# Optimization experiments

Hardware: AMD Instinct MI355X
Metric: run time of the kernel (lower is better)

## Reference

```python
import jax, jax.numpy as jnp
import numpy as np

DIM = 768
HEADS = 8
HIDDEN = 3072
B, Hs, Ws = 16, 32, 32
N = Hs * Ws
LN_EPS = 1e-5


def setup_inputs() -> dict:
    key = jax.random.key(0)
    ks = jax.random.split(key, 10)
    s = lambda *sh: 0.02
    return {
        "x": jax.random.normal(ks[0], (B, N, DIM), jnp.float32),
        "Wq": jax.random.normal(ks[1], (DIM, DIM), jnp.float32) * 0.02,
        "temperature": jnp.ones((HEADS, 1, 1), jnp.float32),
        "fc1_w": jax.random.normal(ks[2], (HIDDEN, DIM), jnp.float32) * 0.02,
        "fc1_b": jnp.zeros((HIDDEN,), jnp.float32),
        "dw_w": jax.random.normal(ks[3], (HIDDEN, 1, 3, 3), jnp.float32) * 0.1,
        "dw_b": jnp.zeros((HIDDEN,), jnp.float32),
        "gamma": jnp.ones((HIDDEN,), jnp.float32),
        "fc2_w": jax.random.normal(ks[4], (DIM, HIDDEN), jnp.float32) * 0.02,
        "fc2_b": jnp.zeros((DIM,), jnp.float32),
        "ln_w": jnp.ones((DIM,), jnp.float32),
        "ln_b": jnp.zeros((DIM,), jnp.float32),
        "H": Hs,
        "W": Ws,
    }


def _dwconv(x, w, b, H, W):
    # x: (B, N, hidden) -> depthwise 3x3, pad 1 -> (B, N, hidden)
    Bn, Nn, Ch = x.shape
    img = x.transpose(0, 2, 1).reshape(Bn, Ch, H, W)
    out = jax.lax.conv_general_dilated(
        img, w, window_strides=(1, 1), padding=((1, 1), (1, 1)),
        dimension_numbers=("NCHW", "OIHW", "NCHW"), feature_group_count=Ch)
    out = out + b[None, :, None, None]
    return out.reshape(Bn, Ch, Nn).transpose(0, 2, 1)


def _layernorm(x, w, b):
    mu = x.mean(-1, keepdims=True)
    var = ((x - mu) ** 2).mean(-1, keepdims=True)
    return (x - mu) * jax.lax.rsqrt(var + LN_EPS) * w + b


def reference(x, Wq, temperature, fc1_w, fc1_b, dw_w, dw_b, gamma,
              fc2_w, fc2_b, ln_w, ln_b, H, W):
    # gpd_ratio == active_ratio == 1 -> pre/post scalings cancel
    Bn, Nn, C = x.shape
    h = temperature.shape[0]
    Ch = C // h
    # q/k/v heads: (B, h, N, Ch)
    q = (x @ Wq.T).reshape(Bn, Nn, h, Ch).transpose(0, 2, 1, 3)
    kv = x.reshape(Bn, Nn, h, Ch).transpose(0, 2, 1, 3)
    # channel attention: softmax over N, pool k over Ch, sigmoid gate
    qs = jax.nn.softmax(q, axis=-2).transpose(0, 1, 3, 2)      # (B,h,Ch,N)
    kp = jax.nn.softmax(kv, axis=-2).mean(-1, keepdims=True)    # (B,h,N,1)
    attn = jax.nn.sigmoid(qs @ kp) * temperature                # (B,h,Ch,1)
    # MLP on v (== x after scaling cancels): fc1 -> dwconv residual -> fc2 -> LN
    h1 = x @ fc1_w.T + fc1_b                                    # (B,N,hidden)
    h2 = gamma * _dwconv(h1, dw_w, dw_b, H, W) + h1
    v = _layernorm(h2 @ fc2_w.T + fc2_b, ln_w, ln_b)            # (B,N,C)
    v = v.reshape(Bn, Nn, h, Ch).transpose(0, 2, 1, 3)          # (B,h,N,Ch)
    prod = attn * v.transpose(0, 1, 3, 2)                       # (B,h,Ch,N)
    out = prod.transpose(0, 3, 1, 2).reshape(Bn, Nn, C)
    return out, prod.transpose(0, 1, 3, 2)
```

## Files before the change

### kernel.cpp

```cpp
#include <hip/hip_runtime.h>

#define BATCH 16
#define SEQ   1024
#define DIM   768
#define NHEAD 8
#define CHD   96
#define HID   3072
#define MTOT  (BATCH * SEQ)

using u16 = unsigned short;
typedef __attribute__((ext_vector_type(8))) short bf16x8;
typedef __attribute__((ext_vector_type(4))) float f32x4;

#define AS1 __attribute__((address_space(1)))
#define AS3 __attribute__((address_space(3)))

__device__ inline float bf2f(u16 u) {
    union { unsigned int i; float f; } v; v.i = ((unsigned int)u) << 16; return v.f;
}
__device__ inline u16 f2bf(float f) {
    union { float f; unsigned int i; } v; v.f = f;
    unsigned int r = v.i + 0x7FFFu + ((v.i >> 16) & 1u);
    return (u16)(r >> 16);
}

__device__ inline void gld16(const void* g, void* l) {
    __builtin_amdgcn_global_load_lds((AS1 const void*)g, (AS3 void*)l, 16, 0, 0);
}

template <int BM>
__global__ __launch_bounds__(512) void gemm_p(const u16* __restrict__ A,
                                              const u16* __restrict__ B,
                                              const float* __restrict__ bias,
                                              u16* __restrict__ C1, int N1,
                                              u16* __restrict__ C2,
                                              int M, int N, int K) {
    constexpr int AROUNDS = BM / 128;
    constexpr int GPT = 2 + AROUNDS;
    constexpr int ASLOT = BM * 32;
    constexpr int AFOLD = BM / 2;
    constexpr int NFI = BM / 32;
    __shared__ u16 lds[4 * (ASLOT + 8192)];

    const int tid = threadIdx.x;
    const int lane = tid & 63;
    const int wid = tid >> 6;
    const int wm = (wid >> 2) * (BM / 2);
    const int wn = (wid & 3) << 6;

    const int nwg = gridDim.x;
    const int wg = blockIdx.x;
    const int lid = (wg & 7) * (nwg >> 3) + (wg >> 3);
    const int nbx = N >> 8;
    const int mb = lid / nbx, nb = lid - mb * nbx;
    const int m0 = mb * BM, n0 = nb << 8;

    const int sprow = tid >> 3;
    const int s_l = (tid & 7) ^ (sprow & 7);
    const int sgk = (s_l & 3) << 3;
    const u16* pa = A + (size_t)(m0 + (s_l >> 2) * AFOLD + sprow) * K + sgk;
    const u16* pb = B + (size_t)(n0 + (s_l >> 2) * 128 + sprow) * K + sgk;
    const size_t r64K = (size_t)64 * K;

#define STAGE_A(slot, k0) do {                                        \
    gld16(pa + (k0), &lds[(slot) * (ASLOT + 8192) + tid * 8]);        \
    if (AROUNDS == 2)                                                 \
        gld16(pa + (k0) + r64K,                                       \
              &lds[(slot) * (ASLOT + 8192) + 4096 + tid * 8]);        \
} while (0)
#define STAGE_B(slot, k0) do {                                        \
    gld16(pb + (k0), &lds[(slot) * (ASLOT + 8192) + ASLOT + tid * 8]);\
    gld16(pb + (k0) + r64K,                                           \
          &lds[(slot) * (ASLOT + 8192) + ASLOT + 4096 + tid * 8]);    \
} while (0)

    const int lrow = lane & 15;
    const int kg = lane >> 4;
    const int xA = (((wid >> 2) * 4 + kg) ^ (lrow & 7)) << 3;
    const int xB = (((wn >> 7) * 4 + kg) ^ (lrow & 7)) << 3;
    const int bbase = (wn & 64) + lrow;

    f32x4 acc[NFI][4] = {};

    const int NT = K >> 5;
    STAGE_A(0, 0);  STAGE_B(0, 0);
    STAGE_A(1, 32); STAGE_B(1, 32);
    STAGE_A(2, 64); STAGE_B(2, 64);

    for (int t = 0; t < NT; ++t) {
        const int rem = NT - 1 - t;
        if (rem >= 2) {
            if constexpr (GPT == 4) asm volatile("s_waitcnt vmcnt(8)" ::: "memory");
            else                    asm volatile("s_waitcnt vmcnt(6)" ::: "memory");
        } else if (rem == 1) {
            if constexpr (GPT == 4) asm volatile("s_waitcnt vmcnt(4)" ::: "memory");
            else                    asm volatile("s_waitcnt vmcnt(3)" ::: "memory");
        } else {
            asm volatile("s_waitcnt vmcnt(0)" ::: "memory");
        }
        __builtin_amdgcn_sched_barrier(0);
        __builtin_amdgcn_s_barrier();

        const u16* Ls = &lds[(t & 3) * (ASLOT + 8192)];
        const int k3 = (t + 3) << 5;

        bf16x8 bfr[4], af[NFI / 2];
#pragma unroll
        for (int j = 0; j < 4; ++j)
            bfr[j] = *(const bf16x8*)&Ls[ASLOT + (bbase + j * 16) * 64 + xB];
#pragma unroll
        for (int i = 0; i < NFI / 2; ++i)
            af[i] = *(const bf16x8*)&Ls[(i * 16 + lrow) * 64 + xA];
        if (rem >= 3) STAGE_A((t + 3) & 3, k3);
        asm volatile("s_waitcnt lgkmcnt(0)" ::: "memory");
        __builtin_amdgcn_sched_barrier(0);
        __builtin_amdgcn_s_setprio(1);
#pragma unroll
        for (int i = 0; i < NFI / 2; ++i)
#pragma unroll
            for (int j = 0; j < 4; ++j)
                acc[i][j] = __builtin_amdgcn_mfma_f32_16x16x32_bf16(af[i], bfr[j], acc[i][j], 0, 0, 0);
        __builtin_amdgcn_s_setprio(0);
        __builtin_amdgcn_s_barrier();

        bf16x8 af2[NFI / 2];
#pragma unroll
        for (int i = 0; i < NFI / 2; ++i)
            af2[i] = *(const bf16x8*)&Ls[((i + NFI / 2) * 16 + lrow) * 64 + xA];
        if (rem >= 3) STAGE_B((t + 3) & 3, k3);
        asm volatile("s_waitcnt lgkmcnt(0)" ::: "memory");
        __builtin_amdgcn_sched_barrier(0);
        __builtin_amdgcn_s_setprio(1);
#pragma unroll
        for (int i = 0; i < NFI / 2; ++i)
#pragma unroll
            for (int j = 0; j < 4; ++j)
                acc[i + NFI / 2][j] = __builtin_amdgcn_mfma_f32_16x16x32_bf16(af2[i], bfr[j], acc[i + NFI / 2][j], 0, 0, 0);
        __builtin_amdgcn_s_setprio(0);
    }
#undef STAGE_A
#undef STAGE_B

    const int crow = (lane >> 4) << 2, ccol = lane & 15;
    const int N2 = N - N1;
#pragma unroll
    for (int i = 0; i < NFI; ++i) {
        const int gm = m0 + wm + i * 16 + crow;
#pragma unroll
        for (int j = 0; j < 4; ++j) {
            const int gn = n0 + wn + j * 16 + ccol;
            if (gn < N1) {
                const float bv = bias ? bias[gn] : 0.f;
#pragma unroll
                for (int r = 0; r < 4; ++r)
                    C1[(size_t)(gm + r) * N1 + gn] = f2bf(acc[i][j][r] + bv);
            } else {
#pragma unroll
                for (int r = 0; r < 4; ++r)
                    C2[(size_t)(gm + r) * N2 + gn - N1] = f2bf(acc[i][j][r]);
            }
        }
    }
}

__global__ __launch_bounds__(256) void cvt_all(const float* __restrict__ x,
                                               const float* __restrict__ Wq,
                                               const float* __restrict__ w1,
                                               const float* __restrict__ w2,
                                               u16* __restrict__ xb,
                                               u16* __restrict__ Wqb,
                                               u16* __restrict__ w1b,
                                               u16* __restrict__ w2b) {
    const int E0 = MTOT * DIM / 4;
    const int E1 = E0 + DIM * DIM / 4;
    const int E2 = E1 + HID * DIM / 4;
    const int E3 = E2 + DIM * HID / 4;
    int i = blockIdx.x * 256 + threadIdx.x;
    if (i >= E3) return;
    const float* in; u16* out; int k;
    if (i < E0)      { in = x;  out = xb;  k = i; }
    else if (i < E1) { in = Wq; out = Wqb; k = i - E0; }
    else if (i < E2) { in = w1; out = w1b; k = i - E1; }
    else             { in = w2; out = w2b; k = i - E2; }
    float4 v = reinterpret_cast<const float4*>(in)[k];
    ushort4 o;
    o.x = f2bf(v.x); o.y = f2bf(v.y); o.z = f2bf(v.z); o.w = f2bf(v.w);
    reinterpret_cast<ushort4*>(out)[k] = o;
}

__global__ __launch_bounds__(256) void colsm_stats(const u16* __restrict__ X,
                                                   float* __restrict__ Mo,
                                                   float* __restrict__ So) {
    const int tid = threadIdx.x, lane = tid & 63, chunk = tid >> 6;
    const int b = blockIdx.y;
    const int j = blockIdx.x * 64 + lane;
    const u16* p = X + (size_t)b * SEQ * DIM + j;
    float m = -3.0e38f, s = 0.f;
    const int nEnd = (chunk + 1) << 8;
    for (int n = chunk << 8; n < nEnd; ++n) {
        float raw = bf2f(p[(size_t)n * DIM]);
        float nm = fmaxf(m, raw);
        s = s * __expf(m - nm) + __expf(raw - nm);
        m = nm;
    }
    __shared__ float ms[4][64], ss[4][64];
    ms[chunk][lane] = m; ss[chunk][lane] = s;
    __syncthreads();
    if (tid < 64) {
        float M = fmaxf(fmaxf(ms[0][lane], ms[1][lane]), fmaxf(ms[2][lane], ms[3][lane]));
        float S = ss[0][lane] * __expf(ms[0][lane] - M) + ss[1][lane] * __expf(ms[1][lane] - M) +
                  ss[2][lane] * __expf(ms[2][lane] - M) + ss[3][lane] * __expf(ms[3][lane] - M);
        Mo[b * DIM + j] = M;
        So[b * DIM + j] = S;
    }
}

__global__ __launch_bounds__(256) void kp_k(const u16* __restrict__ x,
                                            const float* __restrict__ Mx,
                                            const float* __restrict__ Sx,
                                            float* __restrict__ kp) {
    const int n = blockIdx.x, b = blockIdx.y, tid = threadIdx.x;
    __shared__ float p[DIM];
    const u16* row = x + ((size_t)b * SEQ + n) * DIM;
#pragma unroll
    for (int q = 0; q < 3; ++q) {
        int j = tid + (q << 8);
        p[j] = __expf(bf2f(row[j]) - Mx[b * DIM + j]) / Sx[b * DIM + j];
    }
    __syncthreads();
    if (tid < NHEAD) {
        float s = 0.f;
        for (int c = 0; c < CHD; ++c) s += p[tid * CHD + c];
        kp[((size_t)b * NHEAD + tid) * SEQ + n] = s * (1.f / (float)CHD);
    }
}

__global__ __launch_bounds__(256) void qattn_k(const u16* __restrict__ Q,
                                               const float* __restrict__ kp,
                                               const float* __restrict__ temp,
                                               float* __restrict__ attnv) {
    const int tid = threadIdx.x, lane = tid & 63, chunk = tid >> 6;
    const int b = blockIdx.y;
    const int j = blockIdx.x * 64 + lane;
    const int h = j / CHD;
    const u16* qp = Q + (size_t)b * SEQ * DIM + j;
    const float* kpp = kp + ((size_t)b * NHEAD + h) * SEQ;
    float m = -3.0e38f, s = 0.f, a = 0.f;
    const int nEnd = (chunk + 1) << 8;
    for (int n = chunk << 8; n < nEnd; ++n) {
        float q = bf2f(qp[(size_t)n * DIM]);
        float nm = fmaxf(m, q);
        float sc = __expf(m - nm), e = __expf(q - nm);
        s = s * sc + e;
        a = a * sc + e * kpp[n];
        m = nm;
    }
    __shared__ float ms[4][64], ss[4][64], as_[4][64];
    ms[chunk][lane] = m; ss[chunk][lane] = s; as_[chunk][lane] = a;
    __syncthreads();
    if (tid < 64) {
        float M = fmaxf(fmaxf(ms[0][lane], ms[1][lane]), fmaxf(ms[2][lane], ms[3][lane]));
        float S = 0.f, A = 0.f;
#pragma unroll
        for (int c = 0; c < 4; ++c) {
            float sc = __expf(ms[c][lane] - M);
            S += ss[c][lane] * sc;
            A += as_[c][lane] * sc;
        }
        float z = A / S;
        attnv[b * DIM + j] = temp[h] / (1.f + __expf(-z));
    }
}

__global__ __launch_bounds__(128) void dwconv_v(const u16* __restrict__ h1,
                                                const float* __restrict__ w,
                                                const float* __restrict__ dwb,
                                                const float* __restrict__ gamma,
                                                u16* __restrict__ h2) {
    const int g = blockIdx.x * 128 + threadIdx.x;
    const int y = blockIdx.y >> 2;
    const int xw0 = (blockIdx.y & 3) << 3;
    const int b = blockIdx.z;
    const int ch0 = g << 3;

    float wreg[8][9], bias2[8];
#pragma unroll
    for (int c = 0; c < 8; ++c) {
        const float gm = gamma[ch0 + c];
#pragma unroll
        for (int k = 0; k < 9; ++k) wreg[c][k] = gm * w[(ch0 + c) * 9 + k];
        wreg[c][4] += 1.0f;
        bias2[c] = gm * dwb[ch0 + c];
    }

    float acc[8][8];
#pragma unroll
    for (int xo = 0; xo < 8; ++xo)
#pragma unroll
        for (int c = 0; c < 8; ++c) acc[xo][c] = bias2[c];

    const u16* base = h1 + (size_t)b * SEQ * HID + ch0;
#pragma unroll
    for (int dy = 0; dy < 3; ++dy) {
        const int yy = y + dy - 1;
        if ((unsigned)yy > 31u) continue;
#pragma unroll
        for (int cr = -1; cr <= 8; ++cr) {
            const int col = xw0 + cr;
            if ((unsigned)col > 31u) continue;
            const uint4 v = *reinterpret_cast<const uint4*>(
                base + (size_t)((yy << 5) + col) * HID);
            float f[8];
            f[0] = bf2f((u16)(v.x & 0xffff)); f[1] = bf2f((u16)(v.x >> 16));
            f[2] = bf2f((u16)(v.y & 0xffff)); f[3] = bf2f((u16)(v.y >> 16));
            f[4] = bf2f((u16)(v.z & 0xffff)); f[5] = bf2f((u16)(v.z >> 16));
            f[6] = bf2f((u16)(v.w & 0xffff)); f[7] = bf2f((u16)(v.w >> 16));
            const int xlo = cr > 0 ? cr - 1 : 0;
            const int xhi = cr < 7 ? cr + 1 : 7;
#pragma unroll
            for (int xo = 0; xo < 8; ++xo) {
                if (xo < xlo || xo > xhi) continue;
                const int dx = cr - xo + 1;
#pragma unroll
                for (int c = 0; c < 8; ++c)
                    acc[xo][c] += f[c] * wreg[c][dy * 3 + dx];
            }
        }
    }

#pragma unroll
    for (int xo = 0; xo < 8; ++xo) {
        const int n = (y << 5) + xw0 + xo;
        uint4 o;
        o.x = (unsigned)f2bf(acc[xo][0]) | ((unsigned)f2bf(acc[xo][1]) << 16);
        o.y = (unsigned)f2bf(acc[xo][2]) | ((unsigned)f2bf(acc[xo][3]) << 16);
        o.z = (unsigned)f2bf(acc[xo][4]) | ((unsigned)f2bf(acc[xo][5]) << 16);
        o.w = (unsigned)f2bf(acc[xo][6]) | ((unsigned)f2bf(acc[xo][7]) << 16);
        *reinterpret_cast<uint4*>(h2 + ((size_t)b * SEQ + n) * HID + ch0) = o;
    }
}

__global__ __launch_bounds__(256) void ln_out_k(const u16* __restrict__ vpre,
                                                const float* __restrict__ lnw,
                                                const float* __restrict__ lnb,
                                                const float* __restrict__ attnv,
                                                float* __restrict__ out,
                                                float* __restrict__ out2) {
    const int n = blockIdx.x, b = blockIdx.y, tid = threadIdx.x;
    __shared__ float red[4];
    const u16* row = vpre + ((size_t)b * SEQ + n) * DIM;
    float v[3];
    float s = 0.f;
#pragma unroll
    for (int q = 0; q < 3; ++q) { v[q] = bf2f(row[tid + (q << 8)]); s += v[q]; }
#pragma unroll
    for (int o = 32; o; o >>= 1) s += __shfl_down(s, o, 64);
    if ((tid & 63) == 0) red[tid >> 6] = s;
    __syncthreads();
    const float mu = (red[0] + red[1] + red[2] + red[3]) * (1.f / (float)DIM);
    __syncthreads();
    float vs = 0.f;
#pragma unroll
    for (int q = 0; q < 3; ++q) { float d = v[q] - mu; vs += d * d; }
#pragma unroll
    for (int o = 32; o; o >>= 1) vs += __shfl_down(vs, o, 64);
    if ((tid & 63) == 0) red[tid >> 6] = vs;
    __syncthreads();
    const float rstd = rsqrtf((red[0] + red[1] + red[2] + red[3]) * (1.f / (float)DIM) + 1e-5f);
    const float* at = attnv + b * DIM;
    float* orow = out + ((size_t)b * SEQ + n) * DIM;
#pragma unroll
    for (int q = 0; q < 3; ++q) {
        int j = tid + (q << 8);
        float o = (v[q] - mu) * rstd * lnw[j] + lnb[j];
        o *= at[j];
        orow[j] = o;
        int h = j / CHD, c = j - h * CHD;
        out2[(((size_t)b * NHEAD + h) * SEQ + n) * CHD + c] = o;
    }
}

extern "C" void kernel_launch(void* const* d_in, const int* in_sizes, int n_in,
                              void* d_out, int out_size, void* d_ws, size_t ws_size,
                              hipStream_t stream) {
    const float* x     = (const float*)d_in[0];
    const float* Wq    = (const float*)d_in[1];
    const float* temp  = (const float*)d_in[2];
    const float* fc1w  = (const float*)d_in[3];
    const float* fc1b  = (const float*)d_in[4];
    const float* dww   = (const float*)d_in[5];
    const float* dwb   = (const float*)d_in[6];
    const float* gamma = (const float*)d_in[7];
    const float* fc2w  = (const float*)d_in[8];
    const float* fc2b  = (const float*)d_in[9];
    const float* lnw   = (const float*)d_in[10];
    const float* lnb   = (const float*)d_in[11];

    float* out  = (float*)d_out;
    float* out2 = out + (size_t)BATCH * SEQ * DIM;

    char* ws = (char*)d_ws;
    u16* xb     = (u16*)ws;
    u16* h1     = (u16*)(ws + 25165824);
    u16* Bbig   = (u16*)(ws + 125829120);
    u16* Wqb    = Bbig + (size_t)HID * DIM;
    u16* fc2wb  = (u16*)(ws + 131727360);
    float* Mx   = (float*)(ws + 136445952);
    float* Sx   = Mx + BATCH * DIM;
    float* kp   = Sx + BATCH * DIM;
    float* attnv = kp + BATCH * NHEAD * SEQ;
    u16* vpreb  = xb;

    u16* Qb = (u16*)d_out;
    u16* h2 = (u16*)d_out;

    {
        const int tot4 = (MTOT * DIM + DIM * DIM + HID * DIM + DIM * HID) / 4;
        cvt_all<<<(tot4 + 255) / 256, 256, 0, stream>>>(
            x, Wq, fc1w, fc2w, xb, Wqb, Bbig, fc2wb);
    }

    gemm_p<256><<<(MTOT / 256) * (3840 / 256), 512, 0, stream>>>(
        xb, Bbig, fc1b, h1, HID, Qb, MTOT, HID + DIM, DIM);

    colsm_stats<<<dim3(DIM / 64, BATCH), 256, 0, stream>>>(xb, Mx, Sx);
    kp_k<<<dim3(SEQ, BATCH), 256, 0, stream>>>(xb, Mx, Sx, kp);
    qattn_k<<<dim3(DIM / 64, BATCH), 256, 0, stream>>>(Qb, kp, temp, attnv);

    dwconv_v<<<dim3(3, 128, BATCH), 128, 0, stream>>>(h1, dww, dwb, gamma, h2);
    gemm_p<128><<<(MTOT / 128) * (DIM / 256), 512, 0, stream>>>(
        h2, fc2wb, fc2b, vpreb, DIM, (u16*)nullptr, MTOT, DIM, HID);
    ln_out_k<<<dim3(SEQ, BATCH), 256, 0, stream>>>(vpreb, lnw, lnb, attnv, out, out2);
}
```

Measured before the change: 401.2 us.

## Stage GEMM epilogue through LDS, drop mid-loop barrier, warp-reduce kp, larger fc2 tile

The GEMM epilogue now writes the bf16 results into a swizzled LDS tile and then stores them to global memory as 16-byte vectors, replacing scattered 2-byte stores. The second barrier inside the k-loop is removed, the wait counts are fixed to the BM=256 variant, and the fc2 GEMM now uses BM=256 with half as many workgroups. The kp kernel replaces its shared-memory pass and serial 8-thread sum with a 32-lane shuffle reduction. The risks are an LDS race from the removed barrier, since a slot can be restaged while slower waves still read it, and lower occupancy for fc2 with only 192 workgroups.

New measurement: 377.8 us. 5.8% less time.

```diff
diff --git a/kernel.cpp b/kernel.cpp
--- a/kernel.cpp
+++ b/kernel.cpp
@@ -36,7 +36,6 @@
                                               u16* __restrict__ C2,
                                               int M, int N, int K) {
     constexpr int AROUNDS = BM / 128;
-    constexpr int GPT = 2 + AROUNDS;
     constexpr int ASLOT = BM * 32;
     constexpr int AFOLD = BM / 2;
     constexpr int NFI = BM / 32;
@@ -89,15 +88,9 @@
 
     for (int t = 0; t < NT; ++t) {
         const int rem = NT - 1 - t;
-        if (rem >= 2) {
-            if constexpr (GPT == 4) asm volatile("s_waitcnt vmcnt(8)" ::: "memory");
-            else                    asm volatile("s_waitcnt vmcnt(6)" ::: "memory");
-        } else if (rem == 1) {
-            if constexpr (GPT == 4) asm volatile("s_waitcnt vmcnt(4)" ::: "memory");
-            else                    asm volatile("s_waitcnt vmcnt(3)" ::: "memory");
-        } else {
-            asm volatile("s_waitcnt vmcnt(0)" ::: "memory");
-        }
+        if (rem >= 2)      asm volatile("s_waitcnt vmcnt(8)" ::: "memory");
+        else if (rem == 1) asm volatile("s_waitcnt vmcnt(4)" ::: "memory");
+        else               asm volatile("s_waitcnt vmcnt(0)" ::: "memory");
         __builtin_amdgcn_sched_barrier(0);
         __builtin_amdgcn_s_barrier();
 
@@ -121,7 +114,6 @@
             for (int j = 0; j < 4; ++j)
                 acc[i][j] = __builtin_amdgcn_mfma_f32_16x16x32_bf16(af[i], bfr[j], acc[i][j], 0, 0, 0);
         __builtin_amdgcn_s_setprio(0);
-        __builtin_amdgcn_s_barrier();
 
         bf16x8 af2[NFI / 2];
 #pragma unroll
@@ -141,25 +133,36 @@
 #undef STAGE_A
 #undef STAGE_B
 
+    __builtin_amdgcn_s_barrier();
+    u16* Ct = lds;
     const int crow = (lane >> 4) << 2, ccol = lane & 15;
-    const int N2 = N - N1;
 #pragma unroll
     for (int i = 0; i < NFI; ++i) {
-        const int gm = m0 + wm + i * 16 + crow;
 #pragma unroll
         for (int j = 0; j < 4; ++j) {
-            const int gn = n0 + wn + j * 16 + ccol;
-            if (gn < N1) {
-                const float bv = bias ? bias[gn] : 0.f;
-#pragma unroll
-                for (int r = 0; r < 4; ++r)
-                    C1[(size_t)(gm + r) * N1 + gn] = f2bf(acc[i][j][r] + bv);
-            } else {
-#pragma unroll
-                for (int r = 0; r < 4; ++r)
-                    C2[(size_t)(gm + r) * N2 + gn - N1] = f2bf(acc[i][j][r]);
+            const int col = wn + j * 16 + ccol;
+            const int gn = n0 + col;
+            const float bv = (gn < N1) ? bias[gn] : 0.f;
+#pragma unroll
+            for (int r = 0; r < 4; ++r) {
+                const int row = wm + i * 16 + crow + r;
+                const int slot = (col >> 3) ^ (row & 7);
+                Ct[row * 256 + slot * 8 + (col & 7)] = f2bf(acc[i][j][r] + bv);
             }
         }
+    }
+    __builtin_amdgcn_s_barrier();
+    const int N2 = N - N1;
+#pragma unroll
+    for (int k = 0; k < BM / 16; ++k) {
+        const int c = tid + (k << 9);
+        const int row = c >> 5, s = c & 31;
+        bf16x8 v = *(const bf16x8*)&Ct[row * 256 + ((s ^ (row & 7)) << 3)];
+        const int gm = m0 + row, gnb = n0 + (s << 3);
+        if (gnb < N1)
+            *(bf16x8*)&C1[(size_t)gm * N1 + gnb] = v;
+        else
+            *(bf16x8*)&C2[(size_t)gm * N2 + gnb - N1] = v;
     }
 }
 
@@ -220,19 +223,19 @@
                                             const float* __restrict__ Sx,
                                             float* __restrict__ kp) {
     const int n = blockIdx.x, b = blockIdx.y, tid = threadIdx.x;
-    __shared__ float p[DIM];
     const u16* row = x + ((size_t)b * SEQ + n) * DIM;
+    const int h = tid >> 5, c0 = tid & 31;
+    const float* Mrow = Mx + b * DIM;
+    const float* Srow = Sx + b * DIM;
+    float s = 0.f;
 #pragma unroll
     for (int q = 0; q < 3; ++q) {
-        int j = tid + (q << 8);
-        p[j] = __expf(bf2f(row[j]) - Mx[b * DIM + j]) / Sx[b * DIM + j];
-    }
-    __syncthreads();
-    if (tid < NHEAD) {
-        float s = 0.f;
-        for (int c = 0; c < CHD; ++c) s += p[tid * CHD + c];
-        kp[((size_t)b * NHEAD + tid) * SEQ + n] = s * (1.f / (float)CHD);
-    }
+        const int j = h * CHD + c0 + (q << 5);
+        s += __expf(bf2f(row[j]) - Mrow[j]) / Srow[j];
+    }
+#pragma unroll
+    for (int o = 16; o; o >>= 1) s += __shfl_down(s, o, 32);
+    if (c0 == 0) kp[((size_t)b * NHEAD + h) * SEQ + n] = s * (1.f / (float)CHD);
 }
 
 __global__ __launch_bounds__(256) void qattn_k(const u16* __restrict__ Q,
@@ -428,7 +431,7 @@
     qattn_k<<<dim3(DIM / 64, BATCH), 256, 0, stream>>>(Qb, kp, temp, attnv);
 
     dwconv_v<<<dim3(3, 128, BATCH), 128, 0, stream>>>(h1, dww, dwb, gamma, h2);
-    gemm_p<128><<<(MTOT / 128) * (DIM / 256), 512, 0, stream>>>(
+    gemm_p<256><<<(MTOT / 256) * (DIM / 256), 512, 0, stream>>>(
         h2, fc2wb, fc2b, vpreb, DIM, (u16*)nullptr, MTOT, DIM, HID);
     ln_out_k<<<dim3(SEQ, BATCH), 256, 0, stream>>>(vpreb, lnw, lnb, attnv, out, out2);
 }
```
